# Performance work log

Hardware: AMD Instinct MI355X
Metric: run time of the kernel (lower is better)

Reference implementation:

```python
import jax, jax.numpy as jnp
import numpy as np

EMBED_DIM = 512
NUM_HEADS = 8
HEAD_DIM = EMBED_DIM // NUM_HEADS
SHIFT_INIT = 5.0
EPS = 1e-6


def setup_inputs() -> dict:
    key = jax.random.key(0)
    ks = jax.random.split(key, 8)
    L, N, E = 2048, 4, EMBED_DIM
    query = jax.random.normal(ks[0], (L, N, E), dtype=jnp.float32)
    k_in = jax.random.normal(ks[1], (L, N, E), dtype=jnp.float32)
    v_in = jax.random.normal(ks[2], (L, N, E), dtype=jnp.float32)
    # MultiheadAttention packed projections
    in_proj_weight = jax.random.normal(ks[3], (3 * E, E), dtype=jnp.float32) / np.sqrt(E)
    in_proj_bias = jnp.zeros((3 * E,), dtype=jnp.float32)
    out_proj_weight = jax.random.normal(ks[4], (E, E), dtype=jnp.float32) / np.sqrt(E)
    out_proj_bias = jnp.zeros((E,), dtype=jnp.float32)
    # GeM parameters: p ~ N(1, 0.02), shift = 5
    p = 1.0 + 0.02 * jax.random.normal(ks[5], (E,), dtype=jnp.float32)
    shift = jnp.full((E,), SHIFT_INIT, dtype=jnp.float32)
    return {
        "query": query, "key": k_in, "value": v_in,
        "in_proj_weight": in_proj_weight, "in_proj_bias": in_proj_bias,
        "out_proj_weight": out_proj_weight, "out_proj_bias": out_proj_bias,
        "p": p, "shift": shift,
    }


def reference(query, key, value, in_proj_weight, in_proj_bias,
              out_proj_weight, out_proj_bias, p, shift):
    L, N, E = query.shape
    H, D = NUM_HEADS, HEAD_DIM
    w_q, w_k, w_v = jnp.split(in_proj_weight, 3, axis=0)   # each (E, E)
    b_q, b_k, b_v = jnp.split(in_proj_bias, 3, axis=0)

    def proj(x, w, b):
        # (L, N, E) -> (N, H, L, D)
        y = x @ w.T + b
        return y.reshape(L, N, H, D).transpose(1, 2, 0, 3)

    q = proj(query, w_q, b_q)
    k = proj(key, w_k, b_k)
    v = proj(value, w_v, b_v)

    scale = 1.0 / np.sqrt(D)
    scores = jnp.einsum('nhld,nhsd->nhls', q, k) * scale   # (N,H,L,S)
    attn = jax.nn.softmax(scores, axis=-1)

    # GeM pooling of values: shift -> power p -> weighted mean -> inverse power -> unshift
    p_h = p.reshape(H, D)[None, :, None, :]                # (1,H,1,D)
    shift_h = shift.reshape(H, D)[None, :, None, :]
    v_pos = jnp.maximum(v + shift_h, EPS)                  # keep base positive
    pooled = jnp.einsum('nhls,nhsd->nhld', attn, v_pos ** p_h)
    out_h = jnp.maximum(pooled, EPS) ** (1.0 / p_h) - shift_h  # (N,H,L,D)

    out = out_h.transpose(2, 0, 1, 3).reshape(L, N, E)     # back to (L,N,E)
    out = out @ out_proj_weight.T + out_proj_bias
    return out
```

## Files before the change

kernel.cpp:

```cpp
#include <hip/hip_runtime.h>
#include <hip/hip_bf16.h>

#define E_DIM 512
#define N_BATCH 4
#define L_SEQ 2048
#define N_HEADS 8
#define H_DIM 64
#define N_ROWS (L_SEQ * N_BATCH)
#define EPS_F 1e-6f
#define SC_Q 0.18033688f

typedef __attribute__((ext_vector_type(8))) short bf16x8;
typedef __attribute__((ext_vector_type(8))) _Float16 f16x8;
typedef __attribute__((ext_vector_type(4))) float f32x4;
typedef __attribute__((ext_vector_type(16))) float f32x16;

__device__ __forceinline__ void split2(float f, __hip_bfloat16& h, __hip_bfloat16& l) {
  h = __float2bfloat16(f);
  l = __float2bfloat16(f - __bfloat162float(h));
}

__device__ __forceinline__ unsigned int packf16(float a, float b) {
  union { _Float16 h[2]; unsigned int u; } c;
  c.h[0] = (_Float16)a;
  c.h[1] = (_Float16)b;
  return c.u;
}

__global__ __launch_bounds__(256) void wconv_kernel(
    const float* __restrict__ wio, const float* __restrict__ wo,
    __hip_bfloat16* __restrict__ wiohi, __hip_bfloat16* __restrict__ wiolo,
    __hip_bfloat16* __restrict__ wohi, __hip_bfloat16* __restrict__ wolo) {
  const int g = blockIdx.x * 256 + threadIdx.x;
  const float* src;
  __hip_bfloat16 *dh, *dl;
  int i;
  if (g < 196608) { src = wio; dh = wiohi; dl = wiolo; i = g * 4; }
  else            { src = wo;  dh = wohi;  dl = wolo;  i = (g - 196608) * 4; }
  const float4 f = *(const float4*)(src + i);
  alignas(8) __hip_bfloat16 h[4], l[4];
  split2(f.x, h[0], l[0]); split2(f.y, h[1], l[1]);
  split2(f.z, h[2], l[2]); split2(f.w, h[3], l[3]);
  *(uint2*)(dh + i) = *(const uint2*)h;
  *(uint2*)(dl + i) = *(const uint2*)l;
}

__global__ __launch_bounds__(256, 3) void proj_qkv_kernel(
    const float* __restrict__ xq, const float* __restrict__ xk,
    const float* __restrict__ xv, const __hip_bfloat16* __restrict__ whi,
    const float* __restrict__ bias, const float* __restrict__ pw,
    const float* __restrict__ sw,
    _Float16* __restrict__ qbuf, _Float16* __restrict__ kbuf,
    float* __restrict__ ubuf) {
  __shared__ __hip_bfloat16 Xh[128][40];
  __shared__ __hip_bfloat16 Xl[128][40];
  __shared__ __hip_bfloat16 Wh[128][40];
  const int z = blockIdx.z;
  const int row0 = blockIdx.x * 128;
  const int col0 = blockIdx.y * 128;
  const float* __restrict__ xsrc = (z == 0) ? xq : (z == 1) ? xk : xv;
  const int tid = threadIdx.x;
  const int lane = tid & 63;
  const int wv = tid >> 6;
  const int lidx = lane & 15;
  const int quad = lane >> 4;
  const int srow = tid >> 1;
  const int scol = (tid & 1) * 16;

  f32x4 acc[2][8];
#pragma unroll
  for (int rt = 0; rt < 2; ++rt)
#pragma unroll
    for (int ct = 0; ct < 8; ++ct) acc[rt][ct] = (f32x4){0.f, 0.f, 0.f, 0.f};

  const int ar0 = wv * 32 + lidx;

  for (int kt = 0; kt < 16; ++kt) {
    const int k0 = kt * 32;
    {
      const float* xp = xsrc + (size_t)(row0 + srow) * E_DIM + k0 + scol;
      float f[16];
      *(float4*)&f[0]  = ((const float4*)xp)[0];
      *(float4*)&f[4]  = ((const float4*)xp)[1];
      *(float4*)&f[8]  = ((const float4*)xp)[2];
      *(float4*)&f[12] = ((const float4*)xp)[3];
      alignas(16) __hip_bfloat16 hi[16], lo[16];
#pragma unroll
      for (int j = 0; j < 16; ++j) split2(f[j], hi[j], lo[j]);
      *(uint4*)&Xh[srow][scol]     = ((const uint4*)hi)[0];
      *(uint4*)&Xh[srow][scol + 8] = ((const uint4*)hi)[1];
      *(uint4*)&Xl[srow][scol]     = ((const uint4*)lo)[0];
      *(uint4*)&Xl[srow][scol + 8] = ((const uint4*)lo)[1];
    }
    {
      const size_t wof = (size_t)(z * E_DIM + col0 + srow) * E_DIM + k0 + scol;
      *(uint4*)&Wh[srow][scol]     = ((const uint4*)(whi + wof))[0];
      *(uint4*)&Wh[srow][scol + 8] = ((const uint4*)(whi + wof))[1];
    }
    __syncthreads();

    const bf16x8 ah0 = *(const bf16x8*)&Xh[ar0][quad * 8];
    const bf16x8 ah1 = *(const bf16x8*)&Xh[ar0 + 16][quad * 8];
    const bf16x8 al0 = *(const bf16x8*)&Xl[ar0][quad * 8];
    const bf16x8 al1 = *(const bf16x8*)&Xl[ar0 + 16][quad * 8];
#pragma unroll
    for (int ct = 0; ct < 8; ++ct) {
      const bf16x8 bh = *(const bf16x8*)&Wh[ct * 16 + lidx][quad * 8];
      acc[0][ct] = __builtin_amdgcn_mfma_f32_16x16x32_bf16(ah0, bh, acc[0][ct], 0, 0, 0);
      acc[0][ct] = __builtin_amdgcn_mfma_f32_16x16x32_bf16(al0, bh, acc[0][ct], 0, 0, 0);
      acc[1][ct] = __builtin_amdgcn_mfma_f32_16x16x32_bf16(ah1, bh, acc[1][ct], 0, 0, 0);
      acc[1][ct] = __builtin_amdgcn_mfma_f32_16x16x32_bf16(al1, bh, acc[1][ct], 0, 0, 0);
    }
    __syncthreads();
  }

  if (z < 2) {
    _Float16* __restrict__ dst = (z == 0) ? qbuf : kbuf;
    const float scale = (z == 0) ? SC_Q : 1.0f;
    float bv[8];
#pragma unroll
    for (int ct = 0; ct < 8; ++ct) bv[ct] = bias[z * E_DIM + col0 + ct * 16 + lidx];
#pragma unroll
    for (int rt = 0; rt < 2; ++rt)
#pragma unroll
      for (int ct = 0; ct < 8; ++ct) {
        const int e = col0 + ct * 16 + lidx;
        const int h = e >> 6, d = e & 63;
#pragma unroll
        for (int reg = 0; reg < 4; ++reg) {
          const int R = row0 + wv * 32 + rt * 16 + quad * 4 + reg;
          const int lpos = R >> 2, nb = R & 3;
          dst[(((size_t)nb * N_HEADS + h) * L_SEQ + lpos) * H_DIM + d] =
              (_Float16)((acc[rt][ct][reg] + bv[ct]) * scale);
        }
      }
  } else {
    float bv[8], pv[8], sv[8];
#pragma unroll
    for (int ct = 0; ct < 8; ++ct) {
      const int e = col0 + ct * 16 + lidx;
      bv[ct] = bias[2 * E_DIM + e]; pv[ct] = pw[e]; sv[ct] = sw[e];
    }
#pragma unroll
    for (int rt = 0; rt < 2; ++rt)
#pragma unroll
      for (int ct = 0; ct < 8; ++ct) {
        const int e = col0 + ct * 16 + lidx;
        const int h = e >> 6, d = e & 63;
#pragma unroll
        for (int reg = 0; reg < 4; ++reg) {
          const int R = row0 + wv * 32 + rt * 16 + quad * 4 + reg;
          const int lpos = R >> 2, nb = R & 3;
          const float y = acc[rt][ct][reg] + bv[ct];
          const float vp = fmaxf(y + sv[ct], EPS_F);
          ubuf[(((size_t)nb * N_HEADS + h) * L_SEQ + lpos) * H_DIM + d] =
              __powf(vp, pv[ct]);
        }
      }
  }
}

__global__ __launch_bounds__(256) void transp_kernel(
    const float* __restrict__ u, _Float16* __restrict__ uT) {
  __shared__ float T[64][65];
  const int lt = blockIdx.x, h = blockIdx.y, nb = blockIdx.z;
  const int tid = threadIdx.x;
  const int r = tid >> 2;
  const int cb = (tid & 3) * 16;
  const size_t srcbase = ((size_t)nb * N_HEADS + h) * L_SEQ + lt * 64;
  {
    const float* p = u + (srcbase + r) * H_DIM + cb;
    *(float4*)&T[r][cb + 0]  = ((const float4*)p)[0];
    *(float4*)&T[r][cb + 4]  = ((const float4*)p)[1];
    *(float4*)&T[r][cb + 8]  = ((const float4*)p)[2];
    *(float4*)&T[r][cb + 12] = ((const float4*)p)[3];
  }
  __syncthreads();
  alignas(16) _Float16 hv[16];
#pragma unroll
  for (int j = 0; j < 16; ++j) hv[j] = (_Float16)T[cb + j][r];
  const size_t dst = (((size_t)nb * N_HEADS + h) * H_DIM + r) * L_SEQ + lt * 64 + cb;
  *(uint4*)(uT + dst)     = ((const uint4*)hv)[0];
  *(uint4*)(uT + dst + 8) = ((const uint4*)hv)[1];
}

__global__ __launch_bounds__(128, 2) void attn_kernel(
    const _Float16* __restrict__ qbuf, const _Float16* __restrict__ kbuf,
    const _Float16* __restrict__ uT, const float* __restrict__ pw,
    const float* __restrict__ sw, __hip_bfloat16* __restrict__ ohhi,
    __hip_bfloat16* __restrict__ ohlo) {
  __shared__ _Float16 Ks[64][72];
  __shared__ _Float16 Us[64][72];
  const int qt = blockIdx.x, h = blockIdx.y, nb = blockIdx.z;
  const int q0 = qt * 128;
  const int tid = threadIdx.x;
  const int lane = tid & 63;
  const int wv = tid >> 6;
  const int lm = lane & 31;
  const int kg = lane >> 5;
  const int srow = tid >> 1;
  const int scb = (tid & 1) * 32;
  const size_t headbase = ((size_t)nb * N_HEADS + h) * L_SEQ;
  const size_t dbase = ((size_t)nb * N_HEADS + h) * H_DIM;

  f16x8 bq[2][4];
#pragma unroll
  for (int nt = 0; nt < 2; ++nt)
#pragma unroll
    for (int kc = 0; kc < 4; ++kc)
      bq[nt][kc] = *(const f16x8*)(qbuf +
          (headbase + q0 + wv * 64 + nt * 32 + lm) * H_DIM + kc * 16 + kg * 8);

  f32x16 o[2][2];
  o[0][0] = (f32x16)(0.f); o[0][1] = (f32x16)(0.f);
  o[1][0] = (f32x16)(0.f); o[1][1] = (f32x16)(0.f);
  float lsum[2] = {0.f, 0.f};

  for (int scn = 0; scn < 32; ++scn) {
    const int s0 = scn * 64;
    __syncthreads();
    {
      const _Float16* kp = kbuf + (headbase + s0 + srow) * H_DIM + scb;
      *(uint4*)&Ks[srow][scb + 0]  = ((const uint4*)kp)[0];
      *(uint4*)&Ks[srow][scb + 8]  = ((const uint4*)kp)[1];
      *(uint4*)&Ks[srow][scb + 16] = ((const uint4*)kp)[2];
      *(uint4*)&Ks[srow][scb + 24] = ((const uint4*)kp)[3];
      const _Float16* up = uT + (dbase + srow) * L_SEQ + s0 + scb;
      *(uint4*)&Us[srow][scb + 0]  = ((const uint4*)up)[0];
      *(uint4*)&Us[srow][scb + 8]  = ((const uint4*)up)[1];
      *(uint4*)&Us[srow][scb + 16] = ((const uint4*)up)[2];
      *(uint4*)&Us[srow][scb + 24] = ((const uint4*)up)[3];
    }
    __syncthreads();

    f32x16 sc[2][2];
    sc[0][0] = (f32x16)(0.f); sc[0][1] = (f32x16)(0.f);
    sc[1][0] = (f32x16)(0.f); sc[1][1] = (f32x16)(0.f);
#pragma unroll
    for (int kc = 0; kc < 4; ++kc) {
      const f16x8 ak0 = *(const f16x8*)&Ks[lm][kc * 16 + kg * 8];
      const f16x8 ak1 = *(const f16x8*)&Ks[32 + lm][kc * 16 + kg * 8];
      sc[0][0] = __builtin_amdgcn_mfma_f32_32x32x16_f16(ak0, bq[0][kc], sc[0][0], 0, 0, 0);
      sc[0][1] = __builtin_amdgcn_mfma_f32_32x32x16_f16(ak1, bq[0][kc], sc[0][1], 0, 0, 0);
      sc[1][0] = __builtin_amdgcn_mfma_f32_32x32x16_f16(ak0, bq[1][kc], sc[1][0], 0, 0, 0);
      sc[1][1] = __builtin_amdgcn_mfma_f32_32x32x16_f16(ak1, bq[1][kc], sc[1][1], 0, 0, 0);
    }

    unsigned int P2[2][2][4][2];
#pragma unroll
    for (int nt = 0; nt < 2; ++nt)
#pragma unroll
      for (int mt = 0; mt < 2; ++mt)
#pragma unroll
        for (int g = 0; g < 4; ++g) {
          const float p0 = __builtin_amdgcn_exp2f(sc[nt][mt][4 * g + 0]);
          const float p1 = __builtin_amdgcn_exp2f(sc[nt][mt][4 * g + 1]);
          const float p2 = __builtin_amdgcn_exp2f(sc[nt][mt][4 * g + 2]);
          const float p3 = __builtin_amdgcn_exp2f(sc[nt][mt][4 * g + 3]);
          lsum[nt] += (p0 + p1) + (p2 + p3);
          P2[nt][mt][g][0] = packf16(p0, p1);
          P2[nt][mt][g][1] = packf16(p2, p3);
        }

#pragma unroll
    for (int kc = 0; kc < 4; ++kc) {
      const int mt = kc >> 1;
      const f16x8 au0 = *(const f16x8*)&Us[lm][kc * 16 + kg * 8];
      const f16x8 au1 = *(const f16x8*)&Us[32 + lm][kc * 16 + kg * 8];
#pragma unroll
      for (int nt = 0; nt < 2; ++nt) {
        const int gx = (2 * kc) & 3, gy = (2 * kc + 1) & 3;
        const unsigned int x0 = P2[nt][mt][gx][0], x1 = P2[nt][mt][gx][1];
        const unsigned int y0 = P2[nt][mt][gy][0], y1 = P2[nt][mt][gy][1];
        const unsigned int sA = kg ? x0 : y0, sB = kg ? x1 : y1;
        const unsigned int rA = (unsigned int)__shfl_xor((int)sA, 32);
        const unsigned int rB = (unsigned int)__shfl_xor((int)sB, 32);
        union { unsigned int u[4]; f16x8 v; } bp;
        bp.u[0] = kg ? rA : x0;
        bp.u[1] = kg ? rB : x1;
        bp.u[2] = kg ? y0 : rA;
        bp.u[3] = kg ? y1 : rB;
        o[nt][0] = __builtin_amdgcn_mfma_f32_32x32x16_f16(au0, bp.v, o[nt][0], 0, 0, 0);
        o[nt][1] = __builtin_amdgcn_mfma_f32_32x32x16_f16(au1, bp.v, o[nt][1], 0, 0, 0);
      }
    }
  }

#pragma unroll
  for (int nt = 0; nt < 2; ++nt) {
    const float l = lsum[nt] + __shfl_xor(lsum[nt], 32);
    const float inv = 1.0f / l;
    const int qg = q0 + wv * 64 + nt * 32 + lm;
    const size_t base = ((size_t)qg * N_BATCH + nb) * E_DIM + h * H_DIM;
#pragma unroll
    for (int mt2 = 0; mt2 < 2; ++mt2)
#pragma unroll
      for (int g = 0; g < 4; ++g) {
        alignas(8) __hip_bfloat16 hb[4], lb[4];
#pragma unroll
        for (int i = 0; i < 4; ++i) {
          const int d = mt2 * 32 + 8 * g + 4 * kg + i;
          const int e = h * H_DIM + d;
          const float pooled = o[nt][mt2][4 * g + i] * inv;
          const float val = __powf(fmaxf(pooled, EPS_F), 1.0f / pw[e]) - sw[e];
          split2(val, hb[i], lb[i]);
        }
        const int d0 = mt2 * 32 + 8 * g + 4 * kg;
        *(uint2*)(ohhi + base + d0) = *(const uint2*)hb;
        *(uint2*)(ohlo + base + d0) = *(const uint2*)lb;
      }
  }
}

__global__ __launch_bounds__(256, 4) void out_proj_kernel(
    const __hip_bfloat16* __restrict__ xhi, const __hip_bfloat16* __restrict__ xlo,
    const __hip_bfloat16* __restrict__ whi, const __hip_bfloat16* __restrict__ wlo,
    const float* __restrict__ bias, float* __restrict__ out) {
  __shared__ __hip_bfloat16 Xh[128][40];
  __shared__ __hip_bfloat16 Xl[128][40];
  __shared__ __hip_bfloat16 Wh[64][40];
  __shared__ __hip_bfloat16 Wl[64][40];
  const int row0 = blockIdx.x * 128;
  const int col0 = blockIdx.y * 64;
  const int tid = threadIdx.x;
  const int lane = tid & 63;
  const int wv = tid >> 6;
  const int lidx = lane & 15;
  const int quad = lane >> 4;
  const int srow = tid >> 1;
  const int scol = (tid & 1) * 16;
  const int wrow = tid >> 2;
  const int wcol = (tid & 3) * 8;

  f32x4 acc[2][4];
#pragma unroll
  for (int rt = 0; rt < 2; ++rt)
#pragma unroll
    for (int ct = 0; ct < 4; ++ct) acc[rt][ct] = (f32x4){0.f, 0.f, 0.f, 0.f};

  const int ar0 = wv * 32 + lidx;

  for (int kt = 0; kt < 16; ++kt) {
    const int k0 = kt * 32;
    {
      const size_t xof = (size_t)(row0 + srow) * E_DIM + k0 + scol;
      *(uint4*)&Xh[srow][scol]     = ((const uint4*)(xhi + xof))[0];
      *(uint4*)&Xh[srow][scol + 8] = ((const uint4*)(xhi + xof))[1];
      *(uint4*)&Xl[srow][scol]     = ((const uint4*)(xlo + xof))[0];
      *(uint4*)&Xl[srow][scol + 8] = ((const uint4*)(xlo + xof))[1];
      const size_t wof = (size_t)(col0 + wrow) * E_DIM + k0 + wcol;
      *(uint4*)&Wh[wrow][wcol] = *(const uint4*)(whi + wof);
      *(uint4*)&Wl[wrow][wcol] = *(const uint4*)(wlo + wof);
    }
    __syncthreads();

    const bf16x8 ah0 = *(const bf16x8*)&Xh[ar0][quad * 8];
    const bf16x8 ah1 = *(const bf16x8*)&Xh[ar0 + 16][quad * 8];
    const bf16x8 al0 = *(const bf16x8*)&Xl[ar0][quad * 8];
    const bf16x8 al1 = *(const bf16x8*)&Xl[ar0 + 16][quad * 8];
#pragma unroll
    for (int ct = 0; ct < 4; ++ct) {
      const bf16x8 bh = *(const bf16x8*)&Wh[ct * 16 + lidx][quad * 8];
      const bf16x8 bl = *(const bf16x8*)&Wl[ct * 16 + lidx][quad * 8];
      acc[0][ct] = __builtin_amdgcn_mfma_f32_16x16x32_bf16(ah0, bh, acc[0][ct], 0, 0, 0);
      acc[0][ct] = __builtin_amdgcn_mfma_f32_16x16x32_bf16(al0, bh, acc[0][ct], 0, 0, 0);
      acc[0][ct] = __builtin_amdgcn_mfma_f32_16x16x32_bf16(ah0, bl, acc[0][ct], 0, 0, 0);
      acc[1][ct] = __builtin_amdgcn_mfma_f32_16x16x32_bf16(ah1, bh, acc[1][ct], 0, 0, 0);
      acc[1][ct] = __builtin_amdgcn_mfma_f32_16x16x32_bf16(al1, bh, acc[1][ct], 0, 0, 0);
      acc[1][ct] = __builtin_amdgcn_mfma_f32_16x16x32_bf16(ah1, bl, acc[1][ct], 0, 0, 0);
    }
    __syncthreads();
  }

  float bv[4];
#pragma unroll
  for (int ct = 0; ct < 4; ++ct) bv[ct] = bias[col0 + ct * 16 + lidx];
#pragma unroll
  for (int rt = 0; rt < 2; ++rt)
#pragma unroll
    for (int ct = 0; ct < 4; ++ct) {
      const int c = col0 + ct * 16 + lidx;
#pragma unroll
      for (int reg = 0; reg < 4; ++reg) {
        const int R = row0 + wv * 32 + rt * 16 + quad * 4 + reg;
        out[(size_t)R * E_DIM + c] = acc[rt][ct][reg] + bv[ct];
      }
    }
}

extern "C" void kernel_launch(void* const* d_in, const int* in_sizes, int n_in,
                              void* d_out, int out_size, void* d_ws, size_t ws_size,
                              hipStream_t stream) {
  const float* q_in = (const float*)d_in[0];
  const float* k_in = (const float*)d_in[1];
  const float* v_in = (const float*)d_in[2];
  const float* wio  = (const float*)d_in[3];
  const float* bio  = (const float*)d_in[4];
  const float* wo   = (const float*)d_in[5];
  const float* bo   = (const float*)d_in[6];
  const float* pw   = (const float*)d_in[7];
  const float* sw   = (const float*)d_in[8];

  const size_t NE = (size_t)N_ROWS * E_DIM;
  _Float16* qbuf = (_Float16*)d_ws;
  _Float16* kbuf = qbuf + NE;
  float* ubuf = (float*)(kbuf + NE);
  _Float16* uT = (_Float16*)(ubuf + NE);
  __hip_bfloat16* wiohi = (__hip_bfloat16*)(uT + NE);
  __hip_bfloat16* wiolo = wiohi + 786432;
  __hip_bfloat16* wohi  = wiolo + 786432;
  __hip_bfloat16* wolo  = wohi + 262144;
  __hip_bfloat16* ohhi = (__hip_bfloat16*)ubuf;
  __hip_bfloat16* ohlo = ohhi + NE;

  wconv_kernel<<<dim3(1024), 256, 0, stream>>>(wio, wo, wiohi, wiolo, wohi, wolo);
  proj_qkv_kernel<<<dim3(64, 4, 3), 256, 0, stream>>>(q_in, k_in, v_in, wiohi,
                                                      bio, pw, sw, qbuf, kbuf, ubuf);
  transp_kernel<<<dim3(32, 8, 4), 256, 0, stream>>>(ubuf, uT);
  attn_kernel<<<dim3(16, 8, 4), 128, 0, stream>>>(qbuf, kbuf, uT, pw, sw,
                                                  ohhi, ohlo);
  out_proj_kernel<<<dim3(64, 8), 256, 0, stream>>>(ohhi, ohlo, wohi, wolo,
                                                   bo, (float*)d_out);
}
```

Baseline: 288.5 us.

## Split attention key range across four wave groups with shared-memory reduction

The attention kernel now launches 512 threads per block, and four wave-pair groups each process a quarter of each 256-key chunk. This cuts the outer loop from 32 to 8 iterations and raises the number of waves per block. The partial output accumulators and row sums are combined through a two-step LDS reduction (using an XOR swizzle) before the GeM epilogue. This works because the softmax uses a fixed max-free exp2, so partial sums can simply be added. It exposes four times more waves to hide MFMA and load latency with the same 512 blocks, at the cost of extra LDS, reduction syncs, and register pressure under the 512/4 launch bounds.

```diff
diff --git a/kernel.cpp b/kernel.cpp
--- a/kernel.cpp
+++ b/kernel.cpp
@@ -184,22 +184,29 @@
   *(uint4*)(uT + dst + 8) = ((const uint4*)hv)[1];
 }
 
-__global__ __launch_bounds__(128, 2) void attn_kernel(
+__global__ __launch_bounds__(512, 4) void attn_kernel(
     const _Float16* __restrict__ qbuf, const _Float16* __restrict__ kbuf,
     const _Float16* __restrict__ uT, const float* __restrict__ pw,
     const float* __restrict__ sw, __hip_bfloat16* __restrict__ ohhi,
     __hip_bfloat16* __restrict__ ohlo) {
-  __shared__ _Float16 Ks[64][72];
-  __shared__ _Float16 Us[64][72];
+  __shared__ union {
+    struct { _Float16 Ks[256][72]; _Float16 Us[64][280]; } st;
+    struct { float A[2][64][64]; float B[2][64][64];
+             float lA[2][2][64]; float lB[2][2][64]; } red;
+  } sm;
   const int qt = blockIdx.x, h = blockIdx.y, nb = blockIdx.z;
   const int q0 = qt * 128;
   const int tid = threadIdx.x;
   const int lane = tid & 63;
-  const int wv = tid >> 6;
+  const int w = tid >> 6;
+  const int wv = w & 1;
+  const int sg = w >> 1;
   const int lm = lane & 31;
   const int kg = lane >> 5;
   const int srow = tid >> 1;
   const int scb = (tid & 1) * 32;
+  const int urow = tid >> 3;
+  const int ucb = (tid & 7) * 32;
   const size_t headbase = ((size_t)nb * N_HEADS + h) * L_SEQ;
   const size_t dbase = ((size_t)nb * N_HEADS + h) * H_DIM;
 
@@ -216,30 +223,32 @@
   o[1][0] = (f32x16)(0.f); o[1][1] = (f32x16)(0.f);
   float lsum[2] = {0.f, 0.f};
 
-  for (int scn = 0; scn < 32; ++scn) {
-    const int s0 = scn * 64;
+  for (int it = 0; it < 8; ++it) {
+    const int s0 = it * 256;
     __syncthreads();
     {
       const _Float16* kp = kbuf + (headbase + s0 + srow) * H_DIM + scb;
-      *(uint4*)&Ks[srow][scb + 0]  = ((const uint4*)kp)[0];
-      *(uint4*)&Ks[srow][scb + 8]  = ((const uint4*)kp)[1];
-      *(uint4*)&Ks[srow][scb + 16] = ((const uint4*)kp)[2];
-      *(uint4*)&Ks[srow][scb + 24] = ((const uint4*)kp)[3];
-      const _Float16* up = uT + (dbase + srow) * L_SEQ + s0 + scb;
-      *(uint4*)&Us[srow][scb + 0]  = ((const uint4*)up)[0];
-      *(uint4*)&Us[srow][scb + 8]  = ((const uint4*)up)[1];
-      *(uint4*)&Us[srow][scb + 16] = ((const uint4*)up)[2];
-      *(uint4*)&Us[srow][scb + 24] = ((const uint4*)up)[3];
-    }
-    __syncthreads();
+      *(uint4*)&sm.st.Ks[srow][scb + 0]  = ((const uint4*)kp)[0];
+      *(uint4*)&sm.st.Ks[srow][scb + 8]  = ((const uint4*)kp)[1];
+      *(uint4*)&sm.st.Ks[srow][scb + 16] = ((const uint4*)kp)[2];
+      *(uint4*)&sm.st.Ks[srow][scb + 24] = ((const uint4*)kp)[3];
+      const _Float16* up = uT + (dbase + urow) * L_SEQ + s0 + ucb;
+      *(uint4*)&sm.st.Us[urow][ucb + 0]  = ((const uint4*)up)[0];
+      *(uint4*)&sm.st.Us[urow][ucb + 8]  = ((const uint4*)up)[1];
+      *(uint4*)&sm.st.Us[urow][ucb + 16] = ((const uint4*)up)[2];
+      *(uint4*)&sm.st.Us[urow][ucb + 24] = ((const uint4*)up)[3];
+    }
+    __syncthreads();
+
+    const int sr = sg * 64;
 
     f32x16 sc[2][2];
     sc[0][0] = (f32x16)(0.f); sc[0][1] = (f32x16)(0.f);
     sc[1][0] = (f32x16)(0.f); sc[1][1] = (f32x16)(0.f);
 #pragma unroll
     for (int kc = 0; kc < 4; ++kc) {
-      const f16x8 ak0 = *(const f16x8*)&Ks[lm][kc * 16 + kg * 8];
-      const f16x8 ak1 = *(const f16x8*)&Ks[32 + lm][kc * 16 + kg * 8];
+      const f16x8 ak0 = *(const f16x8*)&sm.st.Ks[sr + lm][kc * 16 + kg * 8];
+      const f16x8 ak1 = *(const f16x8*)&sm.st.Ks[sr + 32 + lm][kc * 16 + kg * 8];
       sc[0][0] = __builtin_amdgcn_mfma_f32_32x32x16_f16(ak0, bq[0][kc], sc[0][0], 0, 0, 0);
       sc[0][1] = __builtin_amdgcn_mfma_f32_32x32x16_f16(ak1, bq[0][kc], sc[0][1], 0, 0, 0);
       sc[1][0] = __builtin_amdgcn_mfma_f32_32x32x16_f16(ak0, bq[1][kc], sc[1][0], 0, 0, 0);
@@ -265,8 +274,8 @@
 #pragma unroll
     for (int kc = 0; kc < 4; ++kc) {
       const int mt = kc >> 1;
-      const f16x8 au0 = *(const f16x8*)&Us[lm][kc * 16 + kg * 8];
-      const f16x8 au1 = *(const f16x8*)&Us[32 + lm][kc * 16 + kg * 8];
+      const f16x8 au0 = *(const f16x8*)&sm.st.Us[lm][sr + kc * 16 + kg * 8];
+      const f16x8 au1 = *(const f16x8*)&sm.st.Us[32 + lm][sr + kc * 16 + kg * 8];
 #pragma unroll
       for (int nt = 0; nt < 2; ++nt) {
         const int gx = (2 * kc) & 3, gy = (2 * kc + 1) & 3;
@@ -285,6 +294,56 @@
       }
     }
   }
+
+  float* redA = &sm.red.A[0][0][0];
+  float* redB = &sm.red.B[0][0][0];
+  float* lrA = &sm.red.lA[0][0][0];
+  float* lrB = &sm.red.lB[0][0][0];
+
+  auto publish = [&](float* dst, float* ldst) {
+#pragma unroll
+    for (int nt = 0; nt < 2; ++nt) {
+      ldst[(wv * 2 + nt) * 64 + lane] = lsum[nt];
+#pragma unroll
+      for (int mt2 = 0; mt2 < 2; ++mt2)
+#pragma unroll
+        for (int g = 0; g < 4; ++g) {
+          const int i4 = ((nt * 2 + mt2) * 4 + g) ^ (lane & 7);
+          float4 v = {o[nt][mt2][4 * g + 0], o[nt][mt2][4 * g + 1],
+                      o[nt][mt2][4 * g + 2], o[nt][mt2][4 * g + 3]};
+          *(float4*)(dst + ((size_t)(wv * 64 + lane)) * 64 + i4 * 4) = v;
+        }
+    }
+  };
+  auto accum = [&](const float* srcp, const float* lsrc) {
+#pragma unroll
+    for (int nt = 0; nt < 2; ++nt) {
+      lsum[nt] += lsrc[(wv * 2 + nt) * 64 + lane];
+#pragma unroll
+      for (int mt2 = 0; mt2 < 2; ++mt2)
+#pragma unroll
+        for (int g = 0; g < 4; ++g) {
+          const int i4 = ((nt * 2 + mt2) * 4 + g) ^ (lane & 7);
+          const float4 v =
+              *(const float4*)(srcp + ((size_t)(wv * 64 + lane)) * 64 + i4 * 4);
+          o[nt][mt2][4 * g + 0] += v.x; o[nt][mt2][4 * g + 1] += v.y;
+          o[nt][mt2][4 * g + 2] += v.z; o[nt][mt2][4 * g + 3] += v.w;
+        }
+    }
+  };
+
+  __syncthreads();
+  if (sg == 1) publish(redA, lrA);
+  if (sg == 3) publish(redB, lrB);
+  __syncthreads();
+  if (sg == 0) accum(redA, lrA);
+  if (sg == 2) {
+    accum(redB, lrB);
+    publish(redB, lrB);
+  }
+  __syncthreads();
+  if (sg != 0) return;
+  accum(redB, lrB);
 
 #pragma unroll
   for (int nt = 0; nt < 2; ++nt) {
@@ -417,7 +476,7 @@
   proj_qkv_kernel<<<dim3(64, 4, 3), 256, 0, stream>>>(q_in, k_in, v_in, wiohi,
                                                       bio, pw, sw, qbuf, kbuf, ubuf);
   transp_kernel<<<dim3(32, 8, 4), 256, 0, stream>>>(ubuf, uT);
-  attn_kernel<<<dim3(16, 8, 4), 128, 0, stream>>>(qbuf, kbuf, uT, pw, sw,
+  attn_kernel<<<dim3(16, 8, 4), 512, 0, stream>>>(qbuf, kbuf, uT, pw, sw,
                                                   ohhi, ohlo);
   out_proj_kernel<<<dim3(64, 8), 256, 0, stream>>>(ohhi, ohlo, wohi, wolo,
                                                    bo, (float*)d_out);
```

New measurement: 449.6 us. 55.8% more time.
